# Performance work log

Hardware: AMD Instinct MI355X
Metric: run time of the kernel (lower is better)

The kernel has to match this reference:

```python
import jax, jax.numpy as jnp
import numpy as np

N, E, C, L, B = 40000, 640000, 128, 3, 64
EPS = 1e-5


def _layer_norm(h, g, b):
    m = h.mean(-1, keepdims=True)
    v = h.var(-1, keepdims=True)
    return (h - m) / jnp.sqrt(v + EPS) * g + b


def setup_inputs() -> dict:
    key = jax.random.key(0)
    ks = jax.random.split(key, 24)
    s = 0.05
    inp = {
        "x": jax.random.normal(ks[0], (N, C), jnp.float32),
        "edge_index": jax.random.randint(ks[1], (2, E), 0, N, dtype=jnp.int32),
        "batch": jnp.sort(jax.random.randint(ks[2], (N,), 0, B, dtype=jnp.int32)),
        # pre-scaler Linear(in=C -> hidden=C)
        "pre_w": jax.random.normal(ks[3], (C, C), jnp.float32) * s,
        "pre_b": jnp.zeros((C,), jnp.float32),
        # per-layer GCNConv weight/bias
        "conv_w": jax.random.normal(ks[4], (L, C, C), jnp.float32) * s,
        "conv_b": jnp.zeros((L, C), jnp.float32),
        # per-layer post-conv LayerNorm (applied for layers 0..L-2)
        "ln_g": jnp.ones((L, C), jnp.float32),
        "ln_b": jnp.zeros((L, C), jnp.float32),
        # per-layer FFN: lin1, lin2, LayerNorm
        "ffn_w1": jax.random.normal(ks[5], (L, C, C), jnp.float32) * s,
        "ffn_b1": jnp.zeros((L, C), jnp.float32),
        "ffn_w2": jax.random.normal(ks[6], (L, C, C), jnp.float32) * s,
        "ffn_b2": jnp.zeros((L, C), jnp.float32),
        "ffn_ln_g": jnp.ones((L, C), jnp.float32),
        "ffn_ln_b": jnp.zeros((L, C), jnp.float32),
        # classifier MLP: Linear(C,C)+ReLU+Linear(C,1)
        "cls_w1": jax.random.normal(ks[7], (C, C), jnp.float32) * s,
        "cls_b1": jnp.zeros((C,), jnp.float32),
        "cls_w2": jax.random.normal(ks[8], (C, 1), jnp.float32) * s,
        "cls_b2": jnp.zeros((1,), jnp.float32),
    }
    return inp


def reference(x, edge_index, batch, pre_w, pre_b, conv_w, conv_b, ln_g, ln_b,
              ffn_w1, ffn_b1, ffn_w2, ffn_b2, ffn_ln_g, ffn_ln_b,
              cls_w1, cls_b1, cls_w2, cls_b2):
    src, dst = edge_index[0], edge_index[1]
    # GCN symmetric normalization with self-loops: deg counts incoming edges + 1
    deg = jax.ops.segment_sum(jnp.ones((E,), x.dtype), dst, num_segments=N) + 1.0
    inv_sqrt = jax.lax.rsqrt(deg)                      # [N]
    norm_e = inv_sqrt[src] * inv_sqrt[dst]             # [E]
    self_norm = inv_sqrt * inv_sqrt                    # [N], 1/deg for self-loop

    h = x @ pre_w + pre_b                              # pre_scaler

    for i in range(L):
        layer_in = h
        hw = h @ conv_w[i]                             # [N,C]
        msg = hw[src] * norm_e[:, None]                # gather + scale [E,C]
        h = jax.ops.segment_sum(msg, dst, num_segments=N)
        h = h + hw * self_norm[:, None] + conv_b[i]    # self-loop + bias
        if i < L - 1:
            h = _layer_norm(h, ln_g[i], ln_b[i])       # norm
            h = jax.nn.relu(h)                         # act (act_first=False)
            h = h + layer_in                           # residual (dropout=0)
            # FFN: lin2(relu(lin1(h))) + h, then norm
            y = jax.nn.relu(h @ ffn_w1[i] + ffn_b1[i]) @ ffn_w2[i] + ffn_b2[i] + h
            h = _layer_norm(y, ffn_ln_g[i], ffn_ln_b[i])

    # global mean pool per graph
    counts = jax.ops.segment_sum(jnp.ones((N,), h.dtype), batch, num_segments=B)
    g = jax.ops.segment_sum(h, batch, num_segments=B) / jnp.maximum(counts, 1.0)[:, None]

    out = jax.nn.relu(g @ cls_w1 + cls_b1) @ cls_w2 + cls_b2   # [B,1]
    return out
```

## Files before the change

### kernel.cpp

```cpp
#include <hip/hip_runtime.h>
#include <hip/hip_fp16.h>
#include <cstdint>
#include <cstddef>

#define N_NODES 40000
#define N_EDGES 640000
#define CH 128
#define NL 3
#define NB 64
#define LN_EPS 1e-5f
#define TSTRIDE 132

typedef short short8 __attribute__((ext_vector_type(8)));
typedef float floatx4 __attribute__((ext_vector_type(4)));

__device__ __forceinline__ unsigned short bf16_rne(float f) {
    unsigned int u = __float_as_uint(f);
    unsigned int r = u + 0x7FFF + ((u >> 16) & 1);
    return (unsigned short)(r >> 16);
}


__global__ void deg_kernel(const int* __restrict__ ei, int* __restrict__ degi) {
    int e = blockIdx.x * 256 + threadIdx.x;
    if (e < N_EDGES) atomicAdd(&degi[ei[N_EDGES + e]], 1);
}

__global__ void scan1_kernel(const int* __restrict__ degi, int* __restrict__ rowptr,
                             int* __restrict__ bsum, float* __restrict__ isq) {
    __shared__ int s[256];
    int t = threadIdx.x;
    int i = blockIdx.x * 256 + t;
    int v = (i < N_NODES) ? degi[i] : 0;
    if (i < N_NODES) isq[i] = rsqrtf((float)v + 1.0f);
    s[t] = v;
    __syncthreads();
    for (int off = 1; off < 256; off <<= 1) {
        int add = (t >= off) ? s[t - off] : 0;
        __syncthreads();
        s[t] += add;
        __syncthreads();
    }
    if (i < N_NODES) rowptr[i + 1] = s[t];
    if (t == 255) bsum[blockIdx.x] = s[255];
}

__global__ void scan2_kernel(int* __restrict__ bsum, int* __restrict__ boff, int nb) {
    __shared__ int s[256];
    int t = threadIdx.x;
    int v = (t < nb) ? bsum[t] : 0;
    s[t] = v;
    __syncthreads();
    for (int off = 1; off < 256; off <<= 1) {
        int add = (t >= off) ? s[t - off] : 0;
        __syncthreads();
        s[t] += add;
        __syncthreads();
    }
    if (t < nb) boff[t] = s[t] - v;
}

__global__ void scan3_kernel(int* __restrict__ rowptr, const int* __restrict__ boff) {
    int i = blockIdx.x * 256 + threadIdx.x;
    if (i < N_NODES) rowptr[i + 1] += boff[blockIdx.x];
    if (i == 0 && blockIdx.x == 0) rowptr[0] = 0;
}

__global__ void fill_csr_kernel(const int* __restrict__ ei, const int* __restrict__ rowptr,
                                int* __restrict__ fill, int* __restrict__ srcs) {
    int e = blockIdx.x * 256 + threadIdx.x;
    if (e < N_EDGES) {
        int s = ei[e];
        int d = ei[N_EDGES + e];
        int pos = atomicAdd(&fill[d], 1);
        srcs[rowptr[d] + pos] = s;
    }
}

__global__ void pack_w_kernel(const float* __restrict__ pre_w, const float* __restrict__ conv_w,
                              const float* __restrict__ ffn_w1, const float* __restrict__ ffn_w2,
                              short* __restrict__ wpk) {
    int idx = blockIdx.x * 256 + threadIdx.x;
    int mat = idx >> 14;
    int e = idx & 16383;
    int k = e >> 7, n = e & 127;
    const float* src;
    switch (mat) {
        case 0: src = pre_w; break;
        case 1: case 2: case 3: src = conv_w + (size_t)(mat - 1) * 16384; break;
        case 4: case 5: src = ffn_w1 + (size_t)(mat - 4) * 16384; break;
        default: src = ffn_w2 + (size_t)(mat - 6) * 16384; break;
    }
    float f = src[e];
    unsigned short h = bf16_rne(f);
    float hf = __uint_as_float((unsigned)h << 16);
    unsigned short l = bf16_rne(f - hf);
    int kk = k >> 5, quad = (k >> 3) & 3, j = k & 7;
    int frag = ((kk * 4 + quad) * 128 + n) * 8 + j;
    wpk[(size_t)mat * 32768 + frag] = (short)h;
    wpk[(size_t)mat * 32768 + 16384 + frag] = (short)l;
}


__device__ __forceinline__ void split8(const float* av, short8& ahi, short8& alo) {
#pragma unroll
    for (int j = 0; j < 8; ++j) {
        unsigned short hb = bf16_rne(av[j]);
        ahi[j] = (short)hb;
        alo[j] = (short)bf16_rne(av[j] - __uint_as_float((unsigned)hb << 16));
    }
}

__device__ __forceinline__ void bload_mfma(const short* __restrict__ bh,
                                           short8 ahi, short8 alo, floatx4* acc) {
    short8 bhi[8], blo[8];
#pragma unroll
    for (int c = 0; c < 8; ++c) {
        bhi[c] = *(const short8*)(bh + c * 128);
        blo[c] = *(const short8*)(bh + 16384 + c * 128);
    }
#pragma unroll
    for (int c = 0; c < 8; ++c) {
        acc[c] = __builtin_amdgcn_mfma_f32_16x16x32_bf16(ahi, bhi[c], acc[c], 0, 0, 0);
        acc[c] = __builtin_amdgcn_mfma_f32_16x16x32_bf16(alo, bhi[c], acc[c], 0, 0, 0);
        acc[c] = __builtin_amdgcn_mfma_f32_16x16x32_bf16(ahi, blo[c], acc[c], 0, 0, 0);
    }
}

template <int VARIANT>
__launch_bounds__(256, 3)
__global__ void gemm_fused(const float* __restrict__ A, const short* __restrict__ W1pk,
                           const float* __restrict__ b1, const short* __restrict__ W2pk,
                           const float* __restrict__ b2, const float* __restrict__ Res,
                           const float* __restrict__ gamma, const float* __restrict__ beta,
                           const short* __restrict__ W3pk,
                           float* __restrict__ OutG, __half* __restrict__ OutC) {
    __shared__ float tbuf[64 * TSTRIDE];
    const int tid = threadIdx.x;
    const int lane = tid & 63;
    const int wv = tid >> 6;
    const int row0 = blockIdx.x * 64 + wv * 16;
    const int m = lane & 15;
    const int quad = lane >> 4;

    floatx4 acc[8];
#pragma unroll
    for (int c = 0; c < 8; ++c) acc[c] = (floatx4){0.f, 0.f, 0.f, 0.f};

    const float* arow = A + (size_t)(row0 + m) * CH + quad * 8;
    float* trow_w = tbuf + (wv * 16) * TSTRIDE;
    const float* trow = tbuf + (wv * 16 + m) * TSTRIDE + quad * 8;
    const int boff = quad * 1024 + m * 8;

#pragma unroll 1
    for (int kk = 0; kk < 4; ++kk) {
        float4 a0 = *(const float4*)(arow + kk * 32);
        float4 a1 = *(const float4*)(arow + kk * 32 + 4);
        float av[8] = {a0.x, a0.y, a0.z, a0.w, a1.x, a1.y, a1.z, a1.w};
        short8 ahi, alo;
        split8(av, ahi, alo);
        bload_mfma(W1pk + kk * 4096 + boff, ahi, alo, acc);
    }

#pragma unroll
    for (int c = 0; c < 8; ++c) {
        int col = c * 16 + m;
        float bv = b1[col];
#pragma unroll
        for (int r = 0; r < 4; ++r) {
            int lrow = quad * 4 + r;
            float v = acc[c][r] + bv;
            if (VARIANT == 1) v = fmaxf(v, 0.f);
            trow_w[lrow * TSTRIDE + col] = v;
            if (VARIANT == 0)
                OutG[(size_t)(row0 + quad * 4 + r) * CH + col] = v;
        }
        acc[c] = (floatx4){0.f, 0.f, 0.f, 0.f};
    }

#pragma unroll 1
    for (int kk = 0; kk < 4; ++kk) {
        float4 t0 = *(const float4*)(trow + kk * 32);
        float4 t1 = *(const float4*)(trow + kk * 32 + 4);
        float av[8] = {t0.x, t0.y, t0.z, t0.w, t1.x, t1.y, t1.z, t1.w};
        short8 ahi, alo;
        split8(av, ahi, alo);
        bload_mfma(W2pk + kk * 4096 + boff, ahi, alo, acc);
    }

    if (VARIANT == 0) {
#pragma unroll
        for (int c = 0; c < 8; ++c) {
            int col = c * 16 + m;
#pragma unroll
            for (int r = 0; r < 4; ++r) {
                int row = row0 + quad * 4 + r;
                OutC[(size_t)row * CH + col] = __float2half(acc[c][r]);
            }
        }
        return;
    }

#pragma unroll
    for (int c = 0; c < 8; ++c) {
        int col = c * 16 + m;
        float bv = b2[col];
#pragma unroll
        for (int r = 0; r < 4; ++r)
            acc[c][r] += bv + Res[(size_t)(row0 + quad * 4 + r) * CH + col];
    }
#pragma unroll
    for (int r = 0; r < 4; ++r) {
        float s = 0.f, q = 0.f;
#pragma unroll
        for (int c = 0; c < 8; ++c) {
            float t = acc[c][r];
            s += t;
            q = fmaf(t, t, q);
        }
#pragma unroll
        for (int msk = 1; msk < 16; msk <<= 1) {
            s += __shfl_xor(s, msk);
            q += __shfl_xor(q, msk);
        }
        float mean = s * (1.f / CH);
        float var = q * (1.f / CH) - mean * mean;
        float rstd = rsqrtf(var + LN_EPS);
        int row = row0 + quad * 4 + r;
        int lrow = quad * 4 + r;
#pragma unroll
        for (int c = 0; c < 8; ++c) {
            int col = c * 16 + m;
            float y = (acc[c][r] - mean) * rstd * gamma[col] + beta[col];
            OutG[(size_t)row * CH + col] = y;
            trow_w[lrow * TSTRIDE + col] = y;
        }
    }
#pragma unroll
    for (int c = 0; c < 8; ++c) acc[c] = (floatx4){0.f, 0.f, 0.f, 0.f};

#pragma unroll 1
    for (int kk = 0; kk < 4; ++kk) {
        float4 t0 = *(const float4*)(trow + kk * 32);
        float4 t1 = *(const float4*)(trow + kk * 32 + 4);
        float av[8] = {t0.x, t0.y, t0.z, t0.w, t1.x, t1.y, t1.z, t1.w};
        short8 ahi, alo;
        split8(av, ahi, alo);
        bload_mfma(W3pk + kk * 4096 + boff, ahi, alo, acc);
    }

#pragma unroll
    for (int c = 0; c < 8; ++c) {
        int col = c * 16 + m;
#pragma unroll
        for (int r = 0; r < 4; ++r) {
            int row = row0 + quad * 4 + r;
            OutC[(size_t)row * CH + col] = __float2half(acc[c][r]);
        }
    }
}

template <int FUSED>
__launch_bounds__(256)
__global__ void agg_kernel(const __half* __restrict__ HW, const int* __restrict__ rowptr,
                           const int* __restrict__ srcs, const float* __restrict__ isq,
                           const float* __restrict__ bias, const float* __restrict__ gamma,
                           const float* __restrict__ beta, float* __restrict__ Hres,
                           float* __restrict__ Out) {
    const int lane = threadIdx.x & 63;
    const int node = blockIdx.x * 4 + (threadIdx.x >> 6);
    const int start = rowptr[node];
    const int end = rowptr[node + 1];

    float ax = 0.f, ay = 0.f;
    for (int base = start; base < end; base += 64) {
        int idx = base + lane;
        int clamped = (idx < end) ? idx : (end - 1);
        int sl = srcs[clamped];
        float wl = isq[sl];
        int cnt = end - base;
        if (cnt > 64) cnt = 64;
        int j = 0;
        for (; j + 8 <= cnt; j += 8) {
            int s[8];
            float w[8];
            float2 v[8];
#pragma unroll
            for (int q = 0; q < 8; ++q) {
                s[q] = __shfl(sl, j + q);
                w[q] = __shfl(wl, j + q);
            }
#pragma unroll
            for (int q = 0; q < 8; ++q)
                v[q] = __half22float2(*(const __half2*)(HW + (size_t)s[q] * CH + lane * 2));
#pragma unroll
            for (int q = 0; q < 8; ++q) {
                ax = fmaf(w[q], v[q].x, ax);
                ay = fmaf(w[q], v[q].y, ay);
            }
        }
        for (; j + 4 <= cnt; j += 4) {
            int s0 = __shfl(sl, j), s1 = __shfl(sl, j + 1);
            int s2 = __shfl(sl, j + 2), s3 = __shfl(sl, j + 3);
            float w0 = __shfl(wl, j), w1 = __shfl(wl, j + 1);
            float w2 = __shfl(wl, j + 2), w3 = __shfl(wl, j + 3);
            float2 v0 = __half22float2(*(const __half2*)(HW + (size_t)s0 * CH + lane * 2));
            float2 v1 = __half22float2(*(const __half2*)(HW + (size_t)s1 * CH + lane * 2));
            float2 v2 = __half22float2(*(const __half2*)(HW + (size_t)s2 * CH + lane * 2));
            float2 v3 = __half22float2(*(const __half2*)(HW + (size_t)s3 * CH + lane * 2));
            ax = fmaf(w0, v0.x, ax); ay = fmaf(w0, v0.y, ay);
            ax = fmaf(w1, v1.x, ax); ay = fmaf(w1, v1.y, ay);
            ax = fmaf(w2, v2.x, ax); ay = fmaf(w2, v2.y, ay);
            ax = fmaf(w3, v3.x, ax); ay = fmaf(w3, v3.y, ay);
        }
        for (; j < cnt; ++j) {
            int s = __shfl(sl, j);
            float w = __shfl(wl, j);
            float2 vf = __half22float2(*(const __half2*)(HW + (size_t)s * CH + lane * 2));
            ax = fmaf(w, vf.x, ax);
            ay = fmaf(w, vf.y, ay);
        }
    }
    float d = isq[node];
    const __half2 hv = *(const __half2*)(HW + (size_t)node * CH + lane * 2);
    float2 hf = __half22float2(hv);
    const float2 bb = *(const float2*)(bias + lane * 2);
    float hx = d * ax + d * d * hf.x + bb.x;
    float hy = d * ay + d * d * hf.y + bb.y;

    if (!FUSED) {
        float2 o; o.x = hx; o.y = hy;
        *(float2*)(Out + (size_t)node * CH + lane * 2) = o;
        return;
    }
    float sum = hx + hy;
    float sq = hx * hx + hy * hy;
    for (int msk = 1; msk < 64; msk <<= 1) {
        sum += __shfl_xor(sum, msk);
        sq += __shfl_xor(sq, msk);
    }
    float mean = sum * (1.f / CH);
    float var = sq * (1.f / CH) - mean * mean;
    float rstd = rsqrtf(var + LN_EPS);
    const float2 gg = *(const float2*)(gamma + lane * 2);
    const float2 be = *(const float2*)(beta + lane * 2);
    float y0 = (hx - mean) * rstd * gg.x + be.x;
    float y1 = (hy - mean) * rstd * gg.y + be.y;
    float2* hp = (float2*)(Hres + (size_t)node * CH + lane * 2);
    float2 rr = *hp;
    float2 o;
    o.x = fmaxf(y0, 0.f) + rr.x;
    o.y = fmaxf(y1, 0.f) + rr.y;
    *hp = o;
}

__launch_bounds__(256)
__global__ void pool_kernel(const float* __restrict__ H, const int* __restrict__ batch,
                            float* __restrict__ g, float* __restrict__ cntf) {
    const int lane = threadIdx.x & 63;
    const int w = blockIdx.x * 4 + (threadIdx.x >> 6);
    const int n0 = w * 16;
    float lx = 0.f, ly = 0.f;
    int run = 0;
    int cur = batch[n0];
    for (int t = 0; t < 16; ++t) {
        int n = n0 + t;
        int b = batch[n];
        if (b != cur) {
            atomicAdd(&g[(size_t)cur * CH + lane * 2], lx);
            atomicAdd(&g[(size_t)cur * CH + lane * 2 + 1], ly);
            if (lane == 0) atomicAdd(&cntf[cur], (float)run);
            lx = ly = 0.f; run = 0; cur = b;
        }
        const float2 v = *(const float2*)(H + (size_t)n * CH + lane * 2);
        lx += v.x; ly += v.y; ++run;
    }
    atomicAdd(&g[(size_t)cur * CH + lane * 2], lx);
    atomicAdd(&g[(size_t)cur * CH + lane * 2 + 1], ly);
    if (lane == 0) atomicAdd(&cntf[cur], (float)run);
}

__launch_bounds__(128)
__global__ void cls_kernel(const float* __restrict__ g, const float* __restrict__ cntf,
                           const float* __restrict__ w1, const float* __restrict__ b1,
                           const float* __restrict__ w2, const float* __restrict__ b2,
                           float* __restrict__ out) {
    __shared__ float gm[CH];
    __shared__ float red[2];
    const int b = blockIdx.x;
    const int t = threadIdx.x;
    float inv = 1.f / fmaxf(cntf[b], 1.f);
    gm[t] = g[(size_t)b * CH + t] * inv;
    __syncthreads();
    float acc = b1[t];
    for (int k = 0; k < CH; ++k) acc = fmaf(gm[k], w1[(size_t)k * CH + t], acc);
    float v = fmaxf(acc, 0.f) * w2[t];
    for (int msk = 1; msk < 64; msk <<= 1) v += __shfl_xor(v, msk);
    if ((t & 63) == 0) red[t >> 6] = v;
    __syncthreads();
    if (t == 0) out[b] = red[0] + red[1] + b2[0];
}


extern "C" void kernel_launch(void* const* d_in, const int* in_sizes, int n_in,
                              void* d_out, int out_size, void* d_ws, size_t ws_size,
                              hipStream_t stream) {
    const float* x      = (const float*)d_in[0];
    const int*   ei     = (const int*)d_in[1];
    const int*   batch  = (const int*)d_in[2];
    const float* pre_w  = (const float*)d_in[3];
    const float* pre_b  = (const float*)d_in[4];
    const float* conv_w = (const float*)d_in[5];
    const float* conv_b = (const float*)d_in[6];
    const float* ln_g   = (const float*)d_in[7];
    const float* ln_b   = (const float*)d_in[8];
    const float* ffn_w1 = (const float*)d_in[9];
    const float* ffn_b1 = (const float*)d_in[10];
    const float* ffn_w2 = (const float*)d_in[11];
    const float* ffn_b2 = (const float*)d_in[12];
    const float* fln_g  = (const float*)d_in[13];
    const float* fln_b  = (const float*)d_in[14];
    const float* cls_w1 = (const float*)d_in[15];
    const float* cls_b1 = (const float*)d_in[16];
    const float* cls_w2 = (const float*)d_in[17];
    const float* cls_b2 = (const float*)d_in[18];

    float* H    = (float*)d_ws;
    float* T    = H + (size_t)N_NODES * CH;
    float* R    = T + (size_t)N_NODES * CH;
    __half* HWh = (__half*)R;
    int*   degi = (int*)(R + (size_t)N_NODES * CH);
    int*   fill = degi + N_NODES;
    float* g    = (float*)(fill + N_NODES);
    float* cntf = g + (size_t)NB * CH;
    float* isq  = cntf + NB;
    int*  rowptr = (int*)(isq + N_NODES);
    int*  bsum   = rowptr + N_NODES + 1;
    int*  boff   = bsum + 256;
    int*  srcs   = boff + 256;
    short* wpk   = (short*)(srcs + N_EDGES);

    const int nb_scan = (N_NODES + 255) / 256;

    hipMemsetAsync(degi, 0, (size_t)(2 * N_NODES + NB * CH + NB) * sizeof(int), stream);

    deg_kernel<<<N_EDGES / 256, 256, 0, stream>>>(ei, degi);
    scan1_kernel<<<nb_scan, 256, 0, stream>>>(degi, rowptr, bsum, isq);
    scan2_kernel<<<1, 256, 0, stream>>>(bsum, boff, nb_scan);
    scan3_kernel<<<nb_scan, 256, 0, stream>>>(rowptr, boff);
    fill_csr_kernel<<<N_EDGES / 256, 256, 0, stream>>>(ei, rowptr, fill, srcs);
    pack_w_kernel<<<8 * 16384 / 256, 256, 0, stream>>>(pre_w, conv_w, ffn_w1, ffn_w2, wpk);

    const int gblk = N_NODES / 64;
    const int lblk = N_NODES / 4;

    gemm_fused<0><<<gblk, 256, 0, stream>>>(x, wpk, pre_b,
                                            wpk + 1 * 32768, nullptr, nullptr,
                                            nullptr, nullptr, nullptr, H, HWh);

    for (int i = 0; i < NL; ++i) {
        if (i < NL - 1) {
            agg_kernel<1><<<lblk, 256, 0, stream>>>(HWh, rowptr, srcs, isq,
                                                    conv_b + (size_t)i * CH,
                                                    ln_g + (size_t)i * CH,
                                                    ln_b + (size_t)i * CH, H, nullptr);
            gemm_fused<1><<<gblk, 256, 0, stream>>>(H, wpk + (size_t)(4 + i) * 32768,
                                                    ffn_b1 + (size_t)i * CH,
                                                    wpk + (size_t)(6 + i) * 32768,
                                                    ffn_b2 + (size_t)i * CH, H,
                                                    fln_g + (size_t)i * CH,
                                                    fln_b + (size_t)i * CH,
                                                    wpk + (size_t)(2 + i) * 32768,
                                                    H, HWh);
        } else {
            agg_kernel<0><<<lblk, 256, 0, stream>>>(HWh, rowptr, srcs, isq,
                                                    conv_b + (size_t)i * CH,
                                                    nullptr, nullptr, nullptr, T);
        }
    }

    pool_kernel<<<N_NODES / 64, 256, 0, stream>>>(T, batch, g, cntf);
    cls_kernel<<<NB, CH, 0, stream>>>(g, cntf, cls_w1, cls_b1, cls_w2, cls_b2,
                                      (float*)d_out);
}
```

Measured before the change: 362.0 us.

## Have each wave compute two 16-row tiles to reuse B fragments in fused GEMM

The fused GEMM kernel now runs 128 threads per block, with each wave handling 32 rows as two 16-row MFMA tiles instead of one. Every loaded weight fragment (hi/lo bf16 split) feeds both tiles, halving weight loads per output row and giving the matrix units more independent work per load. In exchange each wave holds twice as many accumulator registers, and the launch bound drops to a minimum of 2 blocks per CU, so occupancy may fall. Shared-memory A reads also change from float4 loads to scalar-indexed loads.

After: 358.2 us. No clear change (-1.0%).

```diff
diff --git a/kernel.cpp b/kernel.cpp
--- a/kernel.cpp
+++ b/kernel.cpp
@@ -111,8 +111,10 @@
     }
 }
 
-__device__ __forceinline__ void bload_mfma(const short* __restrict__ bh,
-                                           short8 ahi, short8 alo, floatx4* acc) {
+__device__ __forceinline__ void bload_mfma2(const short* __restrict__ bh,
+                                            short8 ahi0, short8 alo0,
+                                            short8 ahi1, short8 alo1,
+                                            floatx4* acc0, floatx4* acc1) {
     short8 bhi[8], blo[8];
 #pragma unroll
     for (int c = 0; c < 8; ++c) {
@@ -121,14 +123,17 @@
     }
 #pragma unroll
     for (int c = 0; c < 8; ++c) {
-        acc[c] = __builtin_amdgcn_mfma_f32_16x16x32_bf16(ahi, bhi[c], acc[c], 0, 0, 0);
-        acc[c] = __builtin_amdgcn_mfma_f32_16x16x32_bf16(alo, bhi[c], acc[c], 0, 0, 0);
-        acc[c] = __builtin_amdgcn_mfma_f32_16x16x32_bf16(ahi, blo[c], acc[c], 0, 0, 0);
+        acc0[c] = __builtin_amdgcn_mfma_f32_16x16x32_bf16(ahi0, bhi[c], acc0[c], 0, 0, 0);
+        acc0[c] = __builtin_amdgcn_mfma_f32_16x16x32_bf16(alo0, bhi[c], acc0[c], 0, 0, 0);
+        acc0[c] = __builtin_amdgcn_mfma_f32_16x16x32_bf16(ahi0, blo[c], acc0[c], 0, 0, 0);
+        acc1[c] = __builtin_amdgcn_mfma_f32_16x16x32_bf16(ahi1, bhi[c], acc1[c], 0, 0, 0);
+        acc1[c] = __builtin_amdgcn_mfma_f32_16x16x32_bf16(alo1, bhi[c], acc1[c], 0, 0, 0);
+        acc1[c] = __builtin_amdgcn_mfma_f32_16x16x32_bf16(ahi1, blo[c], acc1[c], 0, 0, 0);
     }
 }
 
 template <int VARIANT>
-__launch_bounds__(256, 3)
+__launch_bounds__(128, 2)
 __global__ void gemm_fused(const float* __restrict__ A, const short* __restrict__ W1pk,
                            const float* __restrict__ b1, const short* __restrict__ W2pk,
                            const float* __restrict__ b2, const float* __restrict__ Res,
@@ -139,84 +144,103 @@
     const int tid = threadIdx.x;
     const int lane = tid & 63;
     const int wv = tid >> 6;
-    const int row0 = blockIdx.x * 64 + wv * 16;
+    const int row0 = blockIdx.x * 64 + wv * 32;
     const int m = lane & 15;
     const int quad = lane >> 4;
 
-    floatx4 acc[8];
-#pragma unroll
-    for (int c = 0; c < 8; ++c) acc[c] = (floatx4){0.f, 0.f, 0.f, 0.f};
-
-    const float* arow = A + (size_t)(row0 + m) * CH + quad * 8;
-    float* trow_w = tbuf + (wv * 16) * TSTRIDE;
-    const float* trow = tbuf + (wv * 16 + m) * TSTRIDE + quad * 8;
+    floatx4 acc[2][8];
+#pragma unroll
+    for (int t = 0; t < 2; ++t)
+#pragma unroll
+        for (int c = 0; c < 8; ++c) acc[t][c] = (floatx4){0.f, 0.f, 0.f, 0.f};
+
+    const float* arow0 = A + (size_t)(row0 + m) * CH + quad * 8;
+    const float* arow1 = arow0 + (size_t)16 * CH;
+    float* trow_w = tbuf + (wv * 32) * TSTRIDE;
+    const float* trow0 = tbuf + (wv * 32 + m) * TSTRIDE + quad * 8;
+    const float* trow1 = trow0 + 16 * TSTRIDE;
     const int boff = quad * 1024 + m * 8;
 
 #pragma unroll 1
     for (int kk = 0; kk < 4; ++kk) {
-        float4 a0 = *(const float4*)(arow + kk * 32);
-        float4 a1 = *(const float4*)(arow + kk * 32 + 4);
-        float av[8] = {a0.x, a0.y, a0.z, a0.w, a1.x, a1.y, a1.z, a1.w};
-        short8 ahi, alo;
-        split8(av, ahi, alo);
-        bload_mfma(W1pk + kk * 4096 + boff, ahi, alo, acc);
-    }
-
+        float4 a0 = *(const float4*)(arow0 + kk * 32);
+        float4 a1 = *(const float4*)(arow0 + kk * 32 + 4);
+        float4 a2 = *(const float4*)(arow1 + kk * 32);
+        float4 a3 = *(const float4*)(arow1 + kk * 32 + 4);
+        float av0[8] = {a0.x, a0.y, a0.z, a0.w, a1.x, a1.y, a1.z, a1.w};
+        float av1[8] = {a2.x, a2.y, a2.z, a2.w, a3.x, a3.y, a3.z, a3.w};
+        short8 ahi0, alo0, ahi1, alo1;
+        split8(av0, ahi0, alo0);
+        split8(av1, ahi1, alo1);
+        bload_mfma2(W1pk + kk * 4096 + boff, ahi0, alo0, ahi1, alo1, acc[0], acc[1]);
+    }
+
+#pragma unroll
+    for (int t = 0; t < 2; ++t)
 #pragma unroll
     for (int c = 0; c < 8; ++c) {
         int col = c * 16 + m;
         float bv = b1[col];
 #pragma unroll
         for (int r = 0; r < 4; ++r) {
-            int lrow = quad * 4 + r;
-            float v = acc[c][r] + bv;
+            int lrow = t * 16 + quad * 4 + r;
+            float v = acc[t][c][r] + bv;
             if (VARIANT == 1) v = fmaxf(v, 0.f);
             trow_w[lrow * TSTRIDE + col] = v;
             if (VARIANT == 0)
-                OutG[(size_t)(row0 + quad * 4 + r) * CH + col] = v;
-        }
-        acc[c] = (floatx4){0.f, 0.f, 0.f, 0.f};
+                OutG[(size_t)(row0 + lrow) * CH + col] = v;
+        }
+        acc[t][c] = (floatx4){0.f, 0.f, 0.f, 0.f};
     }
 
 #pragma unroll 1
     for (int kk = 0; kk < 4; ++kk) {
-        float4 t0 = *(const float4*)(trow + kk * 32);
-        float4 t1 = *(const float4*)(trow + kk * 32 + 4);
-        float av[8] = {t0.x, t0.y, t0.z, t0.w, t1.x, t1.y, t1.z, t1.w};
-        short8 ahi, alo;
-        split8(av, ahi, alo);
-        bload_mfma(W2pk + kk * 4096 + boff, ahi, alo, acc);
+        float av0[8], av1[8];
+#pragma unroll
+        for (int j = 0; j < 8; ++j) av0[j] = trow0[kk * 32 + j];
+#pragma unroll
+        for (int j = 0; j < 8; ++j) av1[j] = trow1[kk * 32 + j];
+        short8 ahi0, alo0, ahi1, alo1;
+        split8(av0, ahi0, alo0);
+        split8(av1, ahi1, alo1);
+        bload_mfma2(W2pk + kk * 4096 + boff, ahi0, alo0, ahi1, alo1, acc[0], acc[1]);
     }
 
     if (VARIANT == 0) {
+#pragma unroll
+        for (int t = 0; t < 2; ++t)
 #pragma unroll
         for (int c = 0; c < 8; ++c) {
             int col = c * 16 + m;
 #pragma unroll
             for (int r = 0; r < 4; ++r) {
-                int row = row0 + quad * 4 + r;
-                OutC[(size_t)row * CH + col] = __float2half(acc[c][r]);
+                int row = row0 + t * 16 + quad * 4 + r;
+                OutC[(size_t)row * CH + col] = __float2half(acc[t][c][r]);
             }
         }
         return;
     }
 
+#pragma unroll
+    for (int t = 0; t < 2; ++t)
 #pragma unroll
     for (int c = 0; c < 8; ++c) {
         int col = c * 16 + m;
         float bv = b2[col];
 #pragma unroll
         for (int r = 0; r < 4; ++r)
-            acc[c][r] += bv + Res[(size_t)(row0 + quad * 4 + r) * CH + col];
-    }
+            acc[t][c][r] += bv + Res[(size_t)(row0 + t * 16 + quad * 4 + r) * CH + col];
+    }
+#pragma unroll
+    for (int t = 0; t < 2; ++t)
 #pragma unroll
     for (int r = 0; r < 4; ++r) {
         float s = 0.f, q = 0.f;
 #pragma unroll
         for (int c = 0; c < 8; ++c) {
-            float t = acc[c][r];
-            s += t;
-            q = fmaf(t, t, q);
+            float v = acc[t][c][r];
+            s += v;
+            q = fmaf(v, v, q);
         }
 #pragma unroll
         for (int msk = 1; msk < 16; msk <<= 1) {
@@ -226,36 +250,43 @@
         float mean = s * (1.f / CH);
         float var = q * (1.f / CH) - mean * mean;
         float rstd = rsqrtf(var + LN_EPS);
-        int row = row0 + quad * 4 + r;
-        int lrow = quad * 4 + r;
+        int lrow = t * 16 + quad * 4 + r;
+        int row = row0 + lrow;
 #pragma unroll
         for (int c = 0; c < 8; ++c) {
             int col = c * 16 + m;
-            float y = (acc[c][r] - mean) * rstd * gamma[col] + beta[col];
+            float y = (acc[t][c][r] - mean) * rstd * gamma[col] + beta[col];
             OutG[(size_t)row * CH + col] = y;
             trow_w[lrow * TSTRIDE + col] = y;
         }
     }
 #pragma unroll
-    for (int c = 0; c < 8; ++c) acc[c] = (floatx4){0.f, 0.f, 0.f, 0.f};
+    for (int t = 0; t < 2; ++t)
+#pragma unroll
+    for (int c = 0; c < 8; ++c) acc[t][c] = (floatx4){0.f, 0.f, 0.f, 0.f};
 
 #pragma unroll 1
     for (int kk = 0; kk < 4; ++kk) {
-        float4 t0 = *(const float4*)(trow + kk * 32);
-        float4 t1 = *(const float4*)(trow + kk * 32 + 4);
-        float av[8] = {t0.x, t0.y, t0.z, t0.w, t1.x, t1.y, t1.z, t1.w};
-        short8 ahi, alo;
-        split8(av, ahi, alo);
-        bload_mfma(W3pk + kk * 4096 + boff, ahi, alo, acc);
-    }
-
+        float av0[8], av1[8];
+#pragma unroll
+        for (int j = 0; j < 8; ++j) av0[j] = trow0[kk * 32 + j];
+#pragma unroll
+        for (int j = 0; j < 8; ++j) av1[j] = trow1[kk * 32 + j];
+        short8 ahi0, alo0, ahi1, alo1;
+        split8(av0, ahi0, alo0);
+        split8(av1, ahi1, alo1);
+        bload_mfma2(W3pk + kk * 4096 + boff, ahi0, alo0, ahi1, alo1, acc[0], acc[1]);
+    }
+
+#pragma unroll
+    for (int t = 0; t < 2; ++t)
 #pragma unroll
     for (int c = 0; c < 8; ++c) {
         int col = c * 16 + m;
 #pragma unroll
         for (int r = 0; r < 4; ++r) {
-            int row = row0 + quad * 4 + r;
-            OutC[(size_t)row * CH + col] = __float2half(acc[c][r]);
+            int row = row0 + t * 16 + quad * 4 + r;
+            OutC[(size_t)row * CH + col] = __float2half(acc[t][c][r]);
         }
     }
 }
@@ -454,7 +485,7 @@
     const int gblk = N_NODES / 64;
     const int lblk = N_NODES / 4;
 
-    gemm_fused<0><<<gblk, 256, 0, stream>>>(x, wpk, pre_b,
+    gemm_fused<0><<<gblk, 128, 0, stream>>>(x, wpk, pre_b,
                                             wpk + 1 * 32768, nullptr, nullptr,
                                             nullptr, nullptr, nullptr, H, HWh);
 
@@ -464,7 +495,7 @@
                                                     conv_b + (size_t)i * CH,
                                                     ln_g + (size_t)i * CH,
                                                     ln_b + (size_t)i * CH, H, nullptr);
-            gemm_fused<1><<<gblk, 256, 0, stream>>>(H, wpk + (size_t)(4 + i) * 32768,
+            gemm_fused<1><<<gblk, 128, 0, stream>>>(H, wpk + (size_t)(4 + i) * 32768,
                                                     ffn_b1 + (size_t)i * CH,
                                                     wpk + (size_t)(6 + i) * 32768,
                                                     ffn_b2 + (size_t)i * CH, H,
```
